# Kernel optimization log

Measured on AMD Instinct MI355X. Metric: run time of the kernel, lower is better.

The kernel has to match this reference:

```python
import jax, jax.numpy as jnp
import numpy as np

E, D, A, F, K = 512, 1024, 128, 32, 31  # encoder_dim, decoder_dim, attention_dim, location_filters, kernel
B, T = 128, 512


def setup_inputs() -> dict:
    key = jax.random.key(0)
    ks = jax.random.split(key, 9)
    s = lambda *sh: 1.0 / np.sqrt(sh[-1])
    return {
        "encoder_outputs": jax.random.normal(ks[0], (B, T, E), jnp.float32),
        "decoder_state": jax.random.normal(ks[1], (B, D), jnp.float32),
        "prev_attention_weights": jax.random.uniform(ks[2], (B, T), jnp.float32),
        # parameters (torch Linear stores [out, in]; Conv1d [out, in, K])
        "W_enc": jax.random.normal(ks[3], (A, E), jnp.float32) * s(A, E),
        "W_dec": jax.random.normal(ks[4], (A, D), jnp.float32) * s(A, D),
        "conv_w": jax.random.normal(ks[5], (F, 1, K), jnp.float32) * (1.0 / np.sqrt(K)),
        "W_loc": jax.random.normal(ks[6], (A, F), jnp.float32) * s(A, F),
        "W_e": jax.random.normal(ks[7], (1, A), jnp.float32) * s(1, A),
        "b_e": jax.random.normal(ks[8], (1,), jnp.float32) * 0.01,
    }


def reference(encoder_outputs, decoder_state, prev_attention_weights,
              W_enc, W_dec, conv_w, W_loc, W_e, b_e):
    # encoder projection: [B,T,E] @ [E,A] -> [B,T,A]
    enc_p = jnp.einsum('bte,ae->bta', encoder_outputs, W_enc)
    # decoder projection: [B,D] -> [B,1,A]
    dec_p = jnp.einsum('bd,ad->ba', decoder_state, W_dec)[:, None, :]
    # location conv: [B,1,T] * [F,1,K] -> [B,F,T], 'same' padding
    loc = jax.lax.conv_general_dilated(
        prev_attention_weights[:, None, :], conv_w,
        window_strides=(1,), padding=[((K - 1) // 2, (K - 1) // 2)],
        dimension_numbers=('NCH', 'OIH', 'NCH'))
    # [B,F,T] -> [B,T,A]
    loc_p = jnp.einsum('bft,af->bta', loc, W_loc)
    # energies: [B,T]
    energies = jnp.einsum('bta,a->bt', jnp.tanh(enc_p + dec_p + loc_p), W_e[0]) + b_e[0]
    attention_weights = jax.nn.softmax(energies, axis=1)
    # context: [B,T] x [B,T,E] -> [B,E]
    context_vector = jnp.einsum('bt,bte->be', attention_weights, encoder_outputs)
    return context_vector, attention_weights
```

## Files before the change

### kernel.cpp

```cpp
#include <hip/hip_runtime.h>
#include <hip/hip_bf16.h>
#include <math.h>

namespace {
constexpr int EDIM  = 512;
constexpr int DDIM  = 1024;
constexpr int ADIM  = 128;
constexpr int FDIM  = 32;
constexpr int KW    = 31;
constexpr int BATCH = 128;
constexpr int TDIM  = 512;

constexpr int BM  = 64;
constexpr int LDA = 40;

constexpr size_t N_ENC  = (size_t)BATCH * TDIM * EDIM;
constexpr size_t N_WENC = (size_t)ADIM * EDIM;
constexpr size_t N_WLOC = (size_t)ADIM * FDIM;
constexpr size_t N_BF   = N_ENC + N_WENC + N_WLOC;
constexpr size_t WS_NEEDED = N_BF * 2 + (size_t)BATCH * ADIM * 4;

typedef __attribute__((ext_vector_type(8))) short short8;
typedef __attribute__((ext_vector_type(4))) float floatx4;

__device__ __forceinline__ float fast_tanh(float x) {
  x = fminf(9.0f, fmaxf(-9.0f, x));
  float e = __expf(2.0f * x);
  return (e - 1.0f) / (e + 1.0f);
}

__device__ __forceinline__ ushort2 pack_bf16(float x, float y) {
  union { __hip_bfloat162 h; ushort2 u; } cv;
  cv.h = __float22bfloat162_rn(make_float2(x, y));
  return cv.u;
}

__device__ __forceinline__ void stage4(ushort* dst, const float4 v) {
  ushort2 lo = pack_bf16(v.x, v.y);
  ushort2 hi = pack_bf16(v.z, v.w);
  *(ushort4*)dst = make_ushort4(lo.x, lo.y, hi.x, hi.y);
}

__device__ __forceinline__ void async_ld16(const void* g, void* l) {
  __builtin_amdgcn_global_load_lds(
      (const __attribute__((address_space(1))) unsigned int*)g,
      (__attribute__((address_space(3))) unsigned int*)l, 16, 0, 0);
}

__global__ __launch_bounds__(256)
void cvt_kernel(const float* __restrict__ enc, const float* __restrict__ Wenc,
                const float* __restrict__ Wloc, ushort* __restrict__ out) {
  size_t e0 = (size_t)blockIdx.x * 2048 + (size_t)threadIdx.x * 8;
  const float* s;
  size_t off;
  if (e0 < N_ENC) { s = enc; off = e0; }
  else if (e0 < N_ENC + N_WENC) { s = Wenc; off = e0 - N_ENC; }
  else { s = Wloc; off = e0 - (N_ENC + N_WENC); }
  float4 v0 = *(const float4*)(s + off);
  float4 v1 = *(const float4*)(s + off + 4);
  union { ushort2 u[4]; short8 v; } o;
  o.u[0] = pack_bf16(v0.x, v0.y); o.u[1] = pack_bf16(v0.z, v0.w);
  o.u[2] = pack_bf16(v1.x, v1.y); o.u[3] = pack_bf16(v1.z, v1.w);
  *(short8*)(out + e0) = o.v;
}

__global__ __launch_bounds__(256)
void dec_proj_kernel(const float* __restrict__ dec,
                     const float* __restrict__ Wdec,
                     float* __restrict__ dec_p) {
  int b = blockIdx.x, az = blockIdx.y;
  int tid = threadIdx.x;
  int al = tid >> 3, seg = tid & 7;
  int a = az * 32 + al;
  const float* dv = dec + (size_t)b * DDIM;
  const float* wv = Wdec + (size_t)a * DDIM;
  float s = 0.f;
  #pragma unroll 8
  for (int it = 0; it < 32; ++it) {
    int d = it * 32 + seg * 4;
    float4 d4 = *(const float4*)(dv + d);
    float4 w4 = *(const float4*)(wv + d);
    s += d4.x * w4.x + d4.y * w4.y + d4.z * w4.z + d4.w * w4.w;
  }
  s += __shfl_xor(s, 1, 64);
  s += __shfl_xor(s, 2, 64);
  s += __shfl_xor(s, 4, 64);
  if (seg == 0) dec_p[b * ADIM + a] = s;
}

__global__ __launch_bounds__(256)
void energies_mfma_kernel(const ushort* __restrict__ enc16,
                          const ushort* __restrict__ wenc16,
                          const ushort* __restrict__ wloc16,
                          const float* __restrict__ pa,
                          const float* __restrict__ convw,
                          const float* __restrict__ We,
                          const float* __restrict__ be,
                          const float* __restrict__ dec_p,
                          float* __restrict__ energies) {
  __shared__ ushort As[BM * 64];
  __shared__ ushort Bs[ADIM * 64];
  __shared__ float pa_s[96];
  __shared__ float cw_s[FDIM][KW + 2];
  __shared__ float We_s[ADIM];
  __shared__ float dp_s[ADIM];
  __shared__ float epart[2][BM];

  const int tid  = threadIdx.x;
  const int b    = blockIdx.y;
  const int t0   = blockIdx.x * BM;
  const int wave = tid >> 6, lane = tid & 63;
  const int wt = wave >> 1, wa = wave & 1;
  const int lc = lane & 15, lq = lane >> 4;
  const int sw = lc & 7;

  if (tid < 96) {
    int gt = t0 - 15 + tid;
    pa_s[tid] = (gt >= 0 && gt < TDIM) ? pa[b * TDIM + gt] : 0.0f;
  }
  for (int id = tid; id < FDIM * KW; id += 256)
    cw_s[id / KW][id % KW] = convw[id];
  if (tid < ADIM) {
    We_s[tid] = We[tid];
    dp_s[tid] = dec_p[b * ADIM + tid];
  }

  const int iA0 = tid, iA1 = tid + 256;
  const ushort* gA0 = enc16 + (size_t)(b * TDIM + t0 + (iA0 >> 3)) * EDIM
                      + ((iA0 & 7) ^ ((iA0 >> 3) & 7)) * 8;
  const ushort* gA1 = enc16 + (size_t)(b * TDIM + t0 + (iA1 >> 3)) * EDIM
                      + ((iA1 & 7) ^ ((iA1 >> 3) & 7)) * 8;
  ushort* lA0 = As + iA0 * 8;
  ushort* lA1 = As + iA1 * 8;
  const ushort* gB[4];
  ushort* lB[4];
  #pragma unroll
  for (int r = 0; r < 4; ++r) {
    int idx = tid + r * 256;
    int row = idx >> 3, gc = (idx & 7) ^ (row & 7);
    gB[r] = wenc16 + (size_t)row * EDIM + gc * 8;
    lB[r] = Bs + idx * 8;
  }

  floatx4 acc[2][4];
  #pragma unroll
  for (int tt = 0; tt < 2; ++tt)
    #pragma unroll
    for (int aT = 0; aT < 4; ++aT)
      acc[tt][aT] = (floatx4){0.f, 0.f, 0.f, 0.f};

  ushort2 cvp[4];

  for (int kt = 0; kt < 8; ++kt) {
    async_ld16(gA0, lA0); async_ld16(gA1, lA1);
    async_ld16(gB[0], lB[0]); async_ld16(gB[1], lB[1]);
    async_ld16(gB[2], lB[2]); async_ld16(gB[3], lB[3]);
    gA0 += 64; gA1 += 64;
    gB[0] += 64; gB[1] += 64; gB[2] += 64; gB[3] += 64;
    __syncthreads();

    if (kt == 0) {
      int tl = tid >> 2, fg = tid & 3;
      float cv[8];
      #pragma unroll
      for (int n = 0; n < 8; ++n) {
        int f = fg * 8 + n;
        float s = 0.f;
        #pragma unroll
        for (int k = 0; k < KW; ++k) s += pa_s[tl + k] * cw_s[f][k];
        cv[n] = s;
      }
      cvp[0] = pack_bf16(cv[0], cv[1]);
      cvp[1] = pack_bf16(cv[2], cv[3]);
      cvp[2] = pack_bf16(cv[4], cv[5]);
      cvp[3] = pack_bf16(cv[6], cv[7]);
    }

    #pragma unroll
    for (int kk = 0; kk < 2; ++kk) {
      const int cco = ((kk * 4 + lq) ^ sw) * 8;
      short8 af[2], bf[4];
      #pragma unroll
      for (int tt = 0; tt < 2; ++tt)
        af[tt] = *(const short8*)&As[(wt * 32 + tt * 16 + lc) * 64 + cco];
      #pragma unroll
      for (int aT = 0; aT < 4; ++aT)
        bf[aT] = *(const short8*)&Bs[(wa * 64 + aT * 16 + lc) * 64 + cco];
      #pragma unroll
      for (int tt = 0; tt < 2; ++tt)
        #pragma unroll
        for (int aT = 0; aT < 4; ++aT)
          acc[tt][aT] = __builtin_amdgcn_mfma_f32_16x16x32_bf16(
              af[tt], bf[aT], acc[tt][aT], 0, 0, 0);
    }
    __syncthreads();
  }

  {
    int tl = tid >> 2, fg = tid & 3;
    union { ushort2 u[4]; short8 v; } o;
    o.u[0] = cvp[0]; o.u[1] = cvp[1]; o.u[2] = cvp[2]; o.u[3] = cvp[3];
    *(short8*)&As[tl * 64 + (fg ^ (tl & 7)) * 8] = o.v;
    #pragma unroll
    for (int r = 0; r < 2; ++r) {
      int idx = tid + r * 256;
      int row = idx >> 2, gc = idx & 3;
      *(short8*)&Bs[row * 64 + (gc ^ (row & 7)) * 8] =
          *(const short8*)(wloc16 + row * 32 + gc * 8);
    }
    __syncthreads();
    const int cco = (lq ^ sw) * 8;
    short8 af[2], bf[4];
    #pragma unroll
    for (int tt = 0; tt < 2; ++tt)
      af[tt] = *(const short8*)&As[(wt * 32 + tt * 16 + lc) * 64 + cco];
    #pragma unroll
    for (int aT = 0; aT < 4; ++aT)
      bf[aT] = *(const short8*)&Bs[(wa * 64 + aT * 16 + lc) * 64 + cco];
    #pragma unroll
    for (int tt = 0; tt < 2; ++tt)
      #pragma unroll
      for (int aT = 0; aT < 4; ++aT)
        acc[tt][aT] = __builtin_amdgcn_mfma_f32_16x16x32_bf16(
            af[tt], bf[aT], acc[tt][aT], 0, 0, 0);
  }

  float dpv[4], wev[4];
  #pragma unroll
  for (int aT = 0; aT < 4; ++aT) {
    int a = wa * 64 + aT * 16 + lc;
    dpv[aT] = dp_s[a];
    wev[aT] = We_s[a];
  }
  #pragma unroll
  for (int tt = 0; tt < 2; ++tt) {
    float es[4] = {0.f, 0.f, 0.f, 0.f};
    #pragma unroll
    for (int aT = 0; aT < 4; ++aT)
      #pragma unroll
      for (int i = 0; i < 4; ++i)
        es[i] += fast_tanh(acc[tt][aT][i] + dpv[aT]) * wev[aT];
    #pragma unroll
    for (int m = 1; m < 16; m <<= 1)
      #pragma unroll
      for (int i = 0; i < 4; ++i) es[i] += __shfl_xor(es[i], m, 64);
    if (lc == 0)
      #pragma unroll
      for (int i = 0; i < 4; ++i)
        epart[wa][wt * 32 + tt * 16 + lq * 4 + i] = es[i];
  }
  __syncthreads();
  if (tid < BM)
    energies[(size_t)b * TDIM + t0 + tid] = epart[0][tid] + epart[1][tid] + be[0];
}

__global__ __launch_bounds__(256)
void energies_fallback_kernel(const float* __restrict__ enc,
                              const float* __restrict__ Wenc,
                              const float* __restrict__ pa,
                              const float* __restrict__ convw,
                              const float* __restrict__ Wloc,
                              const float* __restrict__ We,
                              const float* __restrict__ be,
                              const float* __restrict__ dec_p,
                              float* __restrict__ energies) {
  __shared__ ushort As[BM][LDA];
  __shared__ ushort Bs[ADIM][LDA];
  __shared__ float pa_s[96];
  __shared__ float cw_s[FDIM][KW + 2];
  __shared__ float We_s[ADIM];
  __shared__ float dp_s[ADIM];
  __shared__ float epart[2][BM];

  const int tid  = threadIdx.x;
  const int b    = blockIdx.y;
  const int t0   = blockIdx.x * BM;
  const int wave = tid >> 6, lane = tid & 63;
  const int wt = wave >> 1, wa = wave & 1;
  const int lc = lane & 15, lq = lane >> 4;

  if (tid < 96) {
    int gt = t0 - 15 + tid;
    pa_s[tid] = (gt >= 0 && gt < TDIM) ? pa[b * TDIM + gt] : 0.0f;
  }
  for (int id = tid; id < FDIM * KW; id += 256)
    cw_s[id / KW][id % KW] = convw[id];
  if (tid < ADIM) {
    We_s[tid] = We[tid];
    dp_s[tid] = dec_p[b * ADIM + tid];
  }

  floatx4 acc[2][4];
  #pragma unroll
  for (int tt = 0; tt < 2; ++tt)
    #pragma unroll
    for (int aT = 0; aT < 4; ++aT)
      acc[tt][aT] = (floatx4){0.f, 0.f, 0.f, 0.f};

  const float* encB = enc + ((size_t)b * TDIM + t0) * EDIM;
  ushort2 cvp[4];

  for (int kt = 0; kt < 17; ++kt) {
    if (kt < 16) {
      const int k0 = kt * 32;
      #pragma unroll
      for (int r = 0; r < 2; ++r) {
        int id = tid + 256 * r;
        int row = id >> 3, c4 = id & 7;
        float4 v = *(const float4*)(encB + (size_t)row * EDIM + k0 + c4 * 4);
        stage4(&As[row][c4 * 4], v);
      }
      #pragma unroll
      for (int r = 0; r < 4; ++r) {
        int id = tid + 256 * r;
        int row = id >> 3, c4 = id & 7;
        float4 v = *(const float4*)(Wenc + (size_t)row * EDIM + k0 + c4 * 4);
        stage4(&Bs[row][c4 * 4], v);
      }
    } else {
      int tl = tid >> 2, fg = tid & 3;
      *(ushort2*)&As[tl][fg * 8 + 0] = cvp[0];
      *(ushort2*)&As[tl][fg * 8 + 2] = cvp[1];
      *(ushort2*)&As[tl][fg * 8 + 4] = cvp[2];
      *(ushort2*)&As[tl][fg * 8 + 6] = cvp[3];
      #pragma unroll
      for (int r = 0; r < 4; ++r) {
        int id = tid + 256 * r;
        int row = id >> 3, c4 = id & 7;
        float4 v = *(const float4*)(Wloc + (size_t)row * FDIM + c4 * 4);
        stage4(&Bs[row][c4 * 4], v);
      }
    }
    __syncthreads();
    if (kt == 0) {
      int tl = tid >> 2, fg = tid & 3;
      float cv[8];
      #pragma unroll
      for (int n = 0; n < 8; ++n) {
        int f = fg * 8 + n;
        float s = 0.f;
        #pragma unroll
        for (int k = 0; k < KW; ++k) s += pa_s[tl + k] * cw_s[f][k];
        cv[n] = s;
      }
      cvp[0] = pack_bf16(cv[0], cv[1]);
      cvp[1] = pack_bf16(cv[2], cv[3]);
      cvp[2] = pack_bf16(cv[4], cv[5]);
      cvp[3] = pack_bf16(cv[6], cv[7]);
    }
    short8 af[2], bf[4];
    #pragma unroll
    for (int tt = 0; tt < 2; ++tt)
      af[tt] = *(const short8*)&As[wt * 32 + tt * 16 + lc][lq * 8];
    #pragma unroll
    for (int aT = 0; aT < 4; ++aT)
      bf[aT] = *(const short8*)&Bs[wa * 64 + aT * 16 + lc][lq * 8];
    #pragma unroll
    for (int tt = 0; tt < 2; ++tt)
      #pragma unroll
      for (int aT = 0; aT < 4; ++aT)
        acc[tt][aT] = __builtin_amdgcn_mfma_f32_16x16x32_bf16(
            af[tt], bf[aT], acc[tt][aT], 0, 0, 0);
    __syncthreads();
  }

  float dpv[4], wev[4];
  #pragma unroll
  for (int aT = 0; aT < 4; ++aT) {
    int a = wa * 64 + aT * 16 + lc;
    dpv[aT] = dp_s[a];
    wev[aT] = We_s[a];
  }
  #pragma unroll
  for (int tt = 0; tt < 2; ++tt) {
    float es[4] = {0.f, 0.f, 0.f, 0.f};
    #pragma unroll
    for (int aT = 0; aT < 4; ++aT)
      #pragma unroll
      for (int i = 0; i < 4; ++i)
        es[i] += fast_tanh(acc[tt][aT][i] + dpv[aT]) * wev[aT];
    #pragma unroll
    for (int m = 1; m < 16; m <<= 1)
      #pragma unroll
      for (int i = 0; i < 4; ++i) es[i] += __shfl_xor(es[i], m, 64);
    if (lc == 0)
      #pragma unroll
      for (int i = 0; i < 4; ++i)
        epart[wa][wt * 32 + tt * 16 + lq * 4 + i] = es[i];
  }
  __syncthreads();
  if (tid < BM)
    energies[(size_t)b * TDIM + t0 + tid] = epart[0][tid] + epart[1][tid] + be[0];
}

__global__ __launch_bounds__(256)
void softmax_kernel(float* __restrict__ attn) {
  int b = blockIdx.x;
  int tid = threadIdx.x;
  float* row = attn + (size_t)b * TDIM;
  float x0 = row[tid], x1 = row[tid + 256];
  float m = fmaxf(x0, x1);
  #pragma unroll
  for (int off = 32; off; off >>= 1) m = fmaxf(m, __shfl_xor(m, off, 64));
  __shared__ float redm[4];
  __shared__ float reds[4];
  int wid = tid >> 6, lane = tid & 63;
  if (lane == 0) redm[wid] = m;
  __syncthreads();
  m = fmaxf(fmaxf(redm[0], redm[1]), fmaxf(redm[2], redm[3]));
  float e0 = __expf(x0 - m), e1 = __expf(x1 - m);
  float s = e0 + e1;
  #pragma unroll
  for (int off = 32; off; off >>= 1) s += __shfl_xor(s, off, 64);
  if (lane == 0) reds[wid] = s;
  __syncthreads();
  s = reds[0] + reds[1] + reds[2] + reds[3];
  float inv = 1.0f / s;
  row[tid] = e0 * inv;
  row[tid + 256] = e1 * inv;
}

__global__ __launch_bounds__(256)
void context_kernel(const float* __restrict__ enc,
                    const float* __restrict__ attn,
                    float* __restrict__ ctx) {
  int e = blockIdx.x * 256 + threadIdx.x;
  int b = blockIdx.y;
  int tc = blockIdx.z * 128;
  const float* w = attn + (size_t)b * TDIM + tc;
  const float* ep = enc + ((size_t)b * TDIM + tc) * EDIM + e;
  float acc = 0.f;
  #pragma unroll 8
  for (int t = 0; t < 128; ++t) acc += w[t] * ep[(size_t)t * EDIM];
  atomicAdd(&ctx[(size_t)b * EDIM + e], acc);
}

}

extern "C" void kernel_launch(void* const* d_in, const int* in_sizes, int n_in,
                              void* d_out, int out_size, void* d_ws, size_t ws_size,
                              hipStream_t stream) {
  const float* enc   = (const float*)d_in[0];
  const float* dec   = (const float*)d_in[1];
  const float* pa    = (const float*)d_in[2];
  const float* Wenc  = (const float*)d_in[3];
  const float* Wdec  = (const float*)d_in[4];
  const float* convw = (const float*)d_in[5];
  const float* Wloc  = (const float*)d_in[6];
  const float* We    = (const float*)d_in[7];
  const float* be    = (const float*)d_in[8];

  float* ctx  = (float*)d_out;
  float* attn = (float*)d_out + BATCH * EDIM;

  hipMemsetAsync(ctx, 0, (size_t)BATCH * EDIM * sizeof(float), stream);

  if (ws_size >= WS_NEEDED) {
    ushort* enc16  = (ushort*)d_ws;
    ushort* wenc16 = enc16 + N_ENC;
    ushort* wloc16 = enc16 + N_ENC + N_WENC;
    float*  dec_p  = (float*)(enc16 + N_BF);

    cvt_kernel<<<(unsigned)((N_BF + 2047) / 2048), 256, 0, stream>>>(
        enc, Wenc, Wloc, enc16);
    dim3 g1(BATCH, 4);
    dec_proj_kernel<<<g1, 256, 0, stream>>>(dec, Wdec, dec_p);
    dim3 g3(TDIM / BM, BATCH);
    energies_mfma_kernel<<<g3, 256, 0, stream>>>(enc16, wenc16, wloc16, pa,
                                                 convw, We, be, dec_p, attn);
  } else {
    float* dec_p = (float*)d_ws;
    dim3 g1(BATCH, 4);
    dec_proj_kernel<<<g1, 256, 0, stream>>>(dec, Wdec, dec_p);
    dim3 g3(TDIM / BM, BATCH);
    energies_fallback_kernel<<<g3, 256, 0, stream>>>(enc, Wenc, pa, convw,
                                                     Wloc, We, be, dec_p, attn);
  }

  softmax_kernel<<<BATCH, 256, 0, stream>>>(attn);

  dim3 g5(EDIM / 256, BATCH, TDIM / 128);
  context_kernel<<<g5, 256, 0, stream>>>(enc, attn, ctx);
}
```

Before: 285.4 us.

## Read bf16 encoder copy in context, double-buffer energies GEMM, fuse prep kernels

The context reduction now reads the bf16 encoder copy produced for the GEMM, halving its memory traffic, and reduces across waves in LDS before atomics. The energies kernel double-buffers async global-to-LDS tiles, computes the location conv before the K loop, and targets higher occupancy. The conversion and decoder projection are merged into one launch. This trades context precision (bf16 inputs) for lower bandwidth.

```diff
diff --git a/kernel.cpp b/kernel.cpp
--- a/kernel.cpp
+++ b/kernel.cpp
@@ -19,6 +19,8 @@
 constexpr size_t N_WLOC = (size_t)ADIM * FDIM;
 constexpr size_t N_BF   = N_ENC + N_WENC + N_WLOC;
 constexpr size_t WS_NEEDED = N_BF * 2 + (size_t)BATCH * ADIM * 4;
+constexpr int CVT_BLOCKS = (int)(N_BF / 2048);
+constexpr int DEC_BLOCKS = BATCH * 4;
 
 typedef __attribute__((ext_vector_type(8))) short short8;
 typedef __attribute__((ext_vector_type(4))) float floatx4;
@@ -35,6 +37,12 @@
   return cv.u;
 }
 
+__device__ __forceinline__ float b2f(short u) {
+  union { unsigned int i; float f; } c;
+  c.i = ((unsigned int)(unsigned short)u) << 16;
+  return c.f;
+}
+
 __device__ __forceinline__ void stage4(ushort* dst, const float4 v) {
   ushort2 lo = pack_bf16(v.x, v.y);
   ushort2 hi = pack_bf16(v.z, v.w);
@@ -48,20 +56,409 @@
 }
 
 __global__ __launch_bounds__(256)
-void cvt_kernel(const float* __restrict__ enc, const float* __restrict__ Wenc,
-                const float* __restrict__ Wloc, ushort* __restrict__ out) {
-  size_t e0 = (size_t)blockIdx.x * 2048 + (size_t)threadIdx.x * 8;
-  const float* s;
-  size_t off;
-  if (e0 < N_ENC) { s = enc; off = e0; }
-  else if (e0 < N_ENC + N_WENC) { s = Wenc; off = e0 - N_ENC; }
-  else { s = Wloc; off = e0 - (N_ENC + N_WENC); }
-  float4 v0 = *(const float4*)(s + off);
-  float4 v1 = *(const float4*)(s + off + 4);
-  union { ushort2 u[4]; short8 v; } o;
-  o.u[0] = pack_bf16(v0.x, v0.y); o.u[1] = pack_bf16(v0.z, v0.w);
-  o.u[2] = pack_bf16(v1.x, v1.y); o.u[3] = pack_bf16(v1.z, v1.w);
-  *(short8*)(out + e0) = o.v;
+void prep_kernel(const float* __restrict__ enc, const float* __restrict__ Wenc,
+                 const float* __restrict__ Wloc, const float* __restrict__ dec,
+                 const float* __restrict__ Wdec, ushort* __restrict__ out16,
+                 float* __restrict__ dec_p) {
+  int bid = blockIdx.x;
+  if (bid < CVT_BLOCKS) {
+    size_t e0 = (size_t)bid * 2048 + (size_t)threadIdx.x * 8;
+    const float* s;
+    size_t off;
+    if (e0 < N_ENC) { s = enc; off = e0; }
+    else if (e0 < N_ENC + N_WENC) { s = Wenc; off = e0 - N_ENC; }
+    else { s = Wloc; off = e0 - (N_ENC + N_WENC); }
+    float4 v0 = *(const float4*)(s + off);
+    float4 v1 = *(const float4*)(s + off + 4);
+    union { ushort2 u[4]; short8 v; } o;
+    o.u[0] = pack_bf16(v0.x, v0.y); o.u[1] = pack_bf16(v0.z, v0.w);
+    o.u[2] = pack_bf16(v1.x, v1.y); o.u[3] = pack_bf16(v1.z, v1.w);
+    *(short8*)(out16 + e0) = o.v;
+  } else {
+    int id = bid - CVT_BLOCKS;
+    int b = id >> 2, az = id & 3;
+    int tid = threadIdx.x;
+    int al = tid >> 3, seg = tid & 7;
+    int a = az * 32 + al;
+    const float* dv = dec + (size_t)b * DDIM;
+    const float* wv = Wdec + (size_t)a * DDIM;
+    float s = 0.f;
+    #pragma unroll 8
+    for (int it = 0; it < 32; ++it) {
+      int d = it * 32 + seg * 4;
+      float4 d4 = *(const float4*)(dv + d);
+      float4 w4 = *(const float4*)(wv + d);
+      s += d4.x * w4.x + d4.y * w4.y + d4.z * w4.z + d4.w * w4.w;
+    }
+    s += __shfl_xor(s, 1, 64);
+    s += __shfl_xor(s, 2, 64);
+    s += __shfl_xor(s, 4, 64);
+    if (seg == 0) dec_p[b * ADIM + a] = s;
+  }
+}
+
+__global__ __launch_bounds__(256, 3)
+void energies_mfma_kernel(const ushort* __restrict__ enc16,
+                          const ushort* __restrict__ wenc16,
+                          const ushort* __restrict__ wloc16,
+                          const float* __restrict__ pa,
+                          const float* __restrict__ convw,
+                          const float* __restrict__ We,
+                          const float* __restrict__ be,
+                          const float* __restrict__ dec_p,
+                          float* __restrict__ energies) {
+  __shared__ ushort lds[24832];
+  float* pa_s  = (float*)(lds + 16384);
+  float* cw_s  = pa_s + 96;
+  float* epart = (float*)(lds + 24576);
+
+  const int tid  = threadIdx.x;
+  const int b    = blockIdx.y;
+  const int t0   = blockIdx.x * BM;
+  const int wave = tid >> 6, lane = tid & 63;
+  const int wt = wave >> 1, wa = wave & 1;
+  const int lc = lane & 15, lq = lane >> 4;
+  const int sw = lc & 7;
+
+  if (tid < 96) {
+    int gt = t0 - 15 + tid;
+    pa_s[tid] = (gt >= 0 && gt < TDIM) ? pa[b * TDIM + gt] : 0.0f;
+  }
+  for (int id = tid; id < FDIM * KW; id += 256)
+    cw_s[(id / KW) * 33 + (id % KW)] = convw[id];
+
+  const int iA0 = tid, iA1 = tid + 256;
+  const ushort* gA0 = enc16 + (size_t)(b * TDIM + t0 + (iA0 >> 3)) * EDIM
+                      + ((iA0 & 7) ^ ((iA0 >> 3) & 7)) * 8;
+  const ushort* gA1 = enc16 + (size_t)(b * TDIM + t0 + (iA1 >> 3)) * EDIM
+                      + ((iA1 & 7) ^ ((iA1 >> 3) & 7)) * 8;
+  ushort* lA0 = lds + iA0 * 8;
+  ushort* lA1 = lds + iA1 * 8;
+  const ushort* gB[4];
+  ushort* lB[4];
+  #pragma unroll
+  for (int r = 0; r < 4; ++r) {
+    int idx = tid + r * 256;
+    int row = idx >> 3, gc = (idx & 7) ^ (row & 7);
+    gB[r] = wenc16 + (size_t)row * EDIM + gc * 8;
+    lB[r] = lds + 8192 + idx * 8;
+  }
+
+  async_ld16(gA0, lA0); async_ld16(gA1, lA1);
+  async_ld16(gB[0], lB[0]); async_ld16(gB[1], lB[1]);
+  async_ld16(gB[2], lB[2]); async_ld16(gB[3], lB[3]);
+  gA0 += 64; gA1 += 64;
+  gB[0] += 64; gB[1] += 64; gB[2] += 64; gB[3] += 64;
+
+  const int wi0 = tid, wi1 = tid + 256;
+  short8 wl0 = *(const short8*)(wloc16 + (wi0 >> 2) * FDIM + (wi0 & 3) * 8);
+  short8 wl1 = *(const short8*)(wloc16 + (wi1 >> 2) * FDIM + (wi1 & 3) * 8);
+
+  __syncthreads();
+
+  const int tl = tid >> 2, fg = tid & 3;
+  union { ushort2 u[4]; short8 v; } cvo;
+  {
+    float cv[8];
+    #pragma unroll
+    for (int n = 0; n < 8; ++n) {
+      int f = fg * 8 + n;
+      float s = 0.f;
+      #pragma unroll
+      for (int k = 0; k < KW; ++k) s += pa_s[tl + k] * cw_s[f * 33 + k];
+      cv[n] = s;
+    }
+    cvo.u[0] = pack_bf16(cv[0], cv[1]);
+    cvo.u[1] = pack_bf16(cv[2], cv[3]);
+    cvo.u[2] = pack_bf16(cv[4], cv[5]);
+    cvo.u[3] = pack_bf16(cv[6], cv[7]);
+  }
+  __syncthreads();
+
+  floatx4 acc[2][4];
+  #pragma unroll
+  for (int tt = 0; tt < 2; ++tt)
+    #pragma unroll
+    for (int aT = 0; aT < 4; ++aT)
+      acc[tt][aT] = (floatx4){0.f, 0.f, 0.f, 0.f};
+
+  for (int kt = 0; kt < 8; ++kt) {
+    if (kt) __syncthreads();
+    const int cur = kt & 1;
+    if (kt < 7) {
+      const int aoff = (cur ^ 1) << 12;
+      const int boff = (cur ^ 1) << 13;
+      async_ld16(gA0, lA0 + aoff); async_ld16(gA1, lA1 + aoff);
+      async_ld16(gB[0], lB[0] + boff); async_ld16(gB[1], lB[1] + boff);
+      async_ld16(gB[2], lB[2] + boff); async_ld16(gB[3], lB[3] + boff);
+      gA0 += 64; gA1 += 64;
+      gB[0] += 64; gB[1] += 64; gB[2] += 64; gB[3] += 64;
+    } else {
+      *(short8*)&lds[tl * 64 + (fg ^ (tl & 7)) * 8] = cvo.v;
+      *(short8*)&lds[8192 + (wi0 >> 2) * 64 + ((wi0 & 3) ^ ((wi0 >> 2) & 7)) * 8] = wl0;
+      *(short8*)&lds[8192 + (wi1 >> 2) * 64 + ((wi1 & 3) ^ ((wi1 >> 2) & 7)) * 8] = wl1;
+    }
+    const ushort* Ab = lds + (cur << 12);
+    const ushort* Bb = lds + 8192 + (cur << 13);
+    #pragma unroll
+    for (int kk = 0; kk < 2; ++kk) {
+      const int cco = ((kk * 4 + lq) ^ sw) * 8;
+      short8 af[2], bf[4];
+      #pragma unroll
+      for (int tt = 0; tt < 2; ++tt)
+        af[tt] = *(const short8*)&Ab[(wt * 32 + tt * 16 + lc) * 64 + cco];
+      #pragma unroll
+      for (int aT = 0; aT < 4; ++aT)
+        bf[aT] = *(const short8*)&Bb[(wa * 64 + aT * 16 + lc) * 64 + cco];
+      #pragma unroll
+      for (int tt = 0; tt < 2; ++tt)
+        #pragma unroll
+        for (int aT = 0; aT < 4; ++aT)
+          acc[tt][aT] = __builtin_amdgcn_mfma_f32_16x16x32_bf16(
+              af[tt], bf[aT], acc[tt][aT], 0, 0, 0);
+    }
+  }
+  __syncthreads();
+
+  {
+    const int cco = (lq ^ sw) * 8;
+    short8 af[2], bf[4];
+    #pragma unroll
+    for (int tt = 0; tt < 2; ++tt)
+      af[tt] = *(const short8*)&lds[(wt * 32 + tt * 16 + lc) * 64 + cco];
+    #pragma unroll
+    for (int aT = 0; aT < 4; ++aT)
+      bf[aT] = *(const short8*)&lds[8192 + (wa * 64 + aT * 16 + lc) * 64 + cco];
+    #pragma unroll
+    for (int tt = 0; tt < 2; ++tt)
+      #pragma unroll
+      for (int aT = 0; aT < 4; ++aT)
+        acc[tt][aT] = __builtin_amdgcn_mfma_f32_16x16x32_bf16(
+            af[tt], bf[aT], acc[tt][aT], 0, 0, 0);
+  }
+
+  float dpv[4], wev[4];
+  #pragma unroll
+  for (int aT = 0; aT < 4; ++aT) {
+    int a = wa * 64 + aT * 16 + lc;
+    dpv[aT] = dec_p[b * ADIM + a];
+    wev[aT] = We[a];
+  }
+  #pragma unroll
+  for (int tt = 0; tt < 2; ++tt) {
+    float es[4] = {0.f, 0.f, 0.f, 0.f};
+    #pragma unroll
+    for (int aT = 0; aT < 4; ++aT)
+      #pragma unroll
+      for (int i = 0; i < 4; ++i)
+        es[i] += fast_tanh(acc[tt][aT][i] + dpv[aT]) * wev[aT];
+    #pragma unroll
+    for (int m = 1; m < 16; m <<= 1)
+      #pragma unroll
+      for (int i = 0; i < 4; ++i) es[i] += __shfl_xor(es[i], m, 64);
+    if (lc == 0)
+      #pragma unroll
+      for (int i = 0; i < 4; ++i)
+        epart[wa * 64 + wt * 32 + tt * 16 + lq * 4 + i] = es[i];
+  }
+  __syncthreads();
+  if (tid < BM)
+    energies[(size_t)b * TDIM + t0 + tid] = epart[tid] + epart[64 + tid] + be[0];
+}
+
+__global__ __launch_bounds__(256)
+void softmax_kernel(float* __restrict__ attn) {
+  int b = blockIdx.x;
+  int tid = threadIdx.x;
+  float* row = attn + (size_t)b * TDIM;
+  float x0 = row[tid], x1 = row[tid + 256];
+  float m = fmaxf(x0, x1);
+  #pragma unroll
+  for (int off = 32; off; off >>= 1) m = fmaxf(m, __shfl_xor(m, off, 64));
+  __shared__ float redm[4];
+  __shared__ float reds[4];
+  int wid = tid >> 6, lane = tid & 63;
+  if (lane == 0) redm[wid] = m;
+  __syncthreads();
+  m = fmaxf(fmaxf(redm[0], redm[1]), fmaxf(redm[2], redm[3]));
+  float e0 = __expf(x0 - m), e1 = __expf(x1 - m);
+  float s = e0 + e1;
+  #pragma unroll
+  for (int off = 32; off; off >>= 1) s += __shfl_xor(s, off, 64);
+  if (lane == 0) reds[wid] = s;
+  __syncthreads();
+  s = reds[0] + reds[1] + reds[2] + reds[3];
+  float inv = 1.0f / s;
+  row[tid] = e0 * inv;
+  row[tid + 256] = e1 * inv;
+}
+
+__global__ __launch_bounds__(256)
+void context_bf16_kernel(const ushort* __restrict__ enc16,
+                         const float* __restrict__ attn,
+                         float* __restrict__ ctx) {
+  __shared__ float red[4][512];
+  const int b = blockIdx.y, tc = blockIdx.x * 128;
+  const int wave = threadIdx.x >> 6, lane = threadIdx.x & 63;
+  float acc[8] = {0.f, 0.f, 0.f, 0.f, 0.f, 0.f, 0.f, 0.f};
+  const float* aw = attn + (size_t)b * TDIM + tc + wave * 32;
+  const ushort* ep = enc16 + ((size_t)b * TDIM + tc + wave * 32) * EDIM + lane * 8;
+  #pragma unroll 2
+  for (int t = 0; t < 32; t += 2) {
+    short8 v0 = *(const short8*)(ep + (size_t)t * EDIM);
+    short8 v1 = *(const short8*)(ep + (size_t)(t + 1) * EDIM);
+    float w0 = aw[t], w1 = aw[t + 1];
+    #pragma unroll
+    for (int j = 0; j < 8; ++j)
+      acc[j] += w0 * b2f(v0[j]) + w1 * b2f(v1[j]);
+  }
+  #pragma unroll
+  for (int j = 0; j < 8; ++j) red[wave][lane * 8 + j] = acc[j];
+  __syncthreads();
+  int e = threadIdx.x * 2;
+  float s0 = red[0][e] + red[1][e] + red[2][e] + red[3][e];
+  float s1 = red[0][e + 1] + red[1][e + 1] + red[2][e + 1] + red[3][e + 1];
+  atomicAdd(&ctx[(size_t)b * EDIM + e], s0);
+  atomicAdd(&ctx[(size_t)b * EDIM + e + 1], s1);
+}
+
+__global__ __launch_bounds__(256)
+void energies_fallback_kernel(const float* __restrict__ enc,
+                              const float* __restrict__ Wenc,
+                              const float* __restrict__ pa,
+                              const float* __restrict__ convw,
+                              const float* __restrict__ Wloc,
+                              const float* __restrict__ We,
+                              const float* __restrict__ be,
+                              const float* __restrict__ dec_p,
+                              float* __restrict__ energies) {
+  __shared__ ushort As[BM][LDA];
+  __shared__ ushort Bs[ADIM][LDA];
+  __shared__ float pa_s[96];
+  __shared__ float cw_s[FDIM][KW + 2];
+  __shared__ float We_s[ADIM];
+  __shared__ float dp_s[ADIM];
+  __shared__ float epart[2][BM];
+
+  const int tid  = threadIdx.x;
+  const int b    = blockIdx.y;
+  const int t0   = blockIdx.x * BM;
+  const int wave = tid >> 6, lane = tid & 63;
+  const int wt = wave >> 1, wa = wave & 1;
+  const int lc = lane & 15, lq = lane >> 4;
+
+  if (tid < 96) {
+    int gt = t0 - 15 + tid;
+    pa_s[tid] = (gt >= 0 && gt < TDIM) ? pa[b * TDIM + gt] : 0.0f;
+  }
+  for (int id = tid; id < FDIM * KW; id += 256)
+    cw_s[id / KW][id % KW] = convw[id];
+  if (tid < ADIM) {
+    We_s[tid] = We[tid];
+    dp_s[tid] = dec_p[b * ADIM + tid];
+  }
+
+  floatx4 acc[2][4];
+  #pragma unroll
+  for (int tt = 0; tt < 2; ++tt)
+    #pragma unroll
+    for (int aT = 0; aT < 4; ++aT)
+      acc[tt][aT] = (floatx4){0.f, 0.f, 0.f, 0.f};
+
+  const float* encB = enc + ((size_t)b * TDIM + t0) * EDIM;
+  ushort2 cvp[4];
+
+  for (int kt = 0; kt < 17; ++kt) {
+    if (kt < 16) {
+      const int k0 = kt * 32;
+      #pragma unroll
+      for (int r = 0; r < 2; ++r) {
+        int id = tid + 256 * r;
+        int row = id >> 3, c4 = id & 7;
+        float4 v = *(const float4*)(encB + (size_t)row * EDIM + k0 + c4 * 4);
+        stage4(&As[row][c4 * 4], v);
+      }
+      #pragma unroll
+      for (int r = 0; r < 4; ++r) {
+        int id = tid + 256 * r;
+        int row = id >> 3, c4 = id & 7;
+        float4 v = *(const float4*)(Wenc + (size_t)row * EDIM + k0 + c4 * 4);
+        stage4(&Bs[row][c4 * 4], v);
+      }
+    } else {
+      int tl = tid >> 2, fg = tid & 3;
+      *(ushort2*)&As[tl][fg * 8 + 0] = cvp[0];
+      *(ushort2*)&As[tl][fg * 8 + 2] = cvp[1];
+      *(ushort2*)&As[tl][fg * 8 + 4] = cvp[2];
+      *(ushort2*)&As[tl][fg * 8 + 6] = cvp[3];
+      #pragma unroll
+      for (int r = 0; r < 4; ++r) {
+        int id = tid + 256 * r;
+        int row = id >> 3, c4 = id & 7;
+        float4 v = *(const float4*)(Wloc + (size_t)row * FDIM + c4 * 4);
+        stage4(&Bs[row][c4 * 4], v);
+      }
+    }
+    __syncthreads();
+    if (kt == 0) {
+      int tl = tid >> 2, fg = tid & 3;
+      float cv[8];
+      #pragma unroll
+      for (int n = 0; n < 8; ++n) {
+        int f = fg * 8 + n;
+        float s = 0.f;
+        #pragma unroll
+        for (int k = 0; k < KW; ++k) s += pa_s[tl + k] * cw_s[f][k];
+        cv[n] = s;
+      }
+      cvp[0] = pack_bf16(cv[0], cv[1]);
+      cvp[1] = pack_bf16(cv[2], cv[3]);
+      cvp[2] = pack_bf16(cv[4], cv[5]);
+      cvp[3] = pack_bf16(cv[6], cv[7]);
+    }
+    short8 af[2], bf[4];
+    #pragma unroll
+    for (int tt = 0; tt < 2; ++tt)
+      af[tt] = *(const short8*)&As[wt * 32 + tt * 16 + lc][lq * 8];
+    #pragma unroll
+    for (int aT = 0; aT < 4; ++aT)
+      bf[aT] = *(const short8*)&Bs[wa * 64 + aT * 16 + lc][lq * 8];
+    #pragma unroll
+    for (int tt = 0; tt < 2; ++tt)
+      #pragma unroll
+      for (int aT = 0; aT < 4; ++aT)
+        acc[tt][aT] = __builtin_amdgcn_mfma_f32_16x16x32_bf16(
+            af[tt], bf[aT], acc[tt][aT], 0, 0, 0);
+    __syncthreads();
+  }
+
+  float dpv[4], wev[4];
+  #pragma unroll
+  for (int aT = 0; aT < 4; ++aT) {
+    int a = wa * 64 + aT * 16 + lc;
+    dpv[aT] = dp_s[a];
+    wev[aT] = We_s[a];
+  }
+  #pragma unroll
+  for (int tt = 0; tt < 2; ++tt) {
+    float es[4] = {0.f, 0.f, 0.f, 0.f};
+    #pragma unroll
+    for (int aT = 0; aT < 4; ++aT)
+      #pragma unroll
+      for (int i = 0; i < 4; ++i)
+        es[i] += fast_tanh(acc[tt][aT][i] + dpv[aT]) * wev[aT];
+    #pragma unroll
+    for (int m = 1; m < 16; m <<= 1)
+      #pragma unroll
+      for (int i = 0; i < 4; ++i) es[i] += __shfl_xor(es[i], m, 64);
+    if (lc == 0)
+      #pragma unroll
+      for (int i = 0; i < 4; ++i)
+        epart[wa][wt * 32 + tt * 16 + lq * 4 + i] = es[i];
+  }
+  __syncthreads();
+  if (tid < BM)
+    energies[(size_t)b * TDIM + t0 + tid] = epart[0][tid] + epart[1][tid] + be[0];
 }
 
 __global__ __launch_bounds__(256)
@@ -89,341 +486,9 @@
 }
 
 __global__ __launch_bounds__(256)
-void energies_mfma_kernel(const ushort* __restrict__ enc16,
-                          const ushort* __restrict__ wenc16,
-                          const ushort* __restrict__ wloc16,
-                          const float* __restrict__ pa,
-                          const float* __restrict__ convw,
-                          const float* __restrict__ We,
-                          const float* __restrict__ be,
-                          const float* __restrict__ dec_p,
-                          float* __restrict__ energies) {
-  __shared__ ushort As[BM * 64];
-  __shared__ ushort Bs[ADIM * 64];
-  __shared__ float pa_s[96];
-  __shared__ float cw_s[FDIM][KW + 2];
-  __shared__ float We_s[ADIM];
-  __shared__ float dp_s[ADIM];
-  __shared__ float epart[2][BM];
-
-  const int tid  = threadIdx.x;
-  const int b    = blockIdx.y;
-  const int t0   = blockIdx.x * BM;
-  const int wave = tid >> 6, lane = tid & 63;
-  const int wt = wave >> 1, wa = wave & 1;
-  const int lc = lane & 15, lq = lane >> 4;
-  const int sw = lc & 7;
-
-  if (tid < 96) {
-    int gt = t0 - 15 + tid;
-    pa_s[tid] = (gt >= 0 && gt < TDIM) ? pa[b * TDIM + gt] : 0.0f;
-  }
-  for (int id = tid; id < FDIM * KW; id += 256)
-    cw_s[id / KW][id % KW] = convw[id];
-  if (tid < ADIM) {
-    We_s[tid] = We[tid];
-    dp_s[tid] = dec_p[b * ADIM + tid];
-  }
-
-  const int iA0 = tid, iA1 = tid + 256;
-  const ushort* gA0 = enc16 + (size_t)(b * TDIM + t0 + (iA0 >> 3)) * EDIM
-                      + ((iA0 & 7) ^ ((iA0 >> 3) & 7)) * 8;
-  const ushort* gA1 = enc16 + (size_t)(b * TDIM + t0 + (iA1 >> 3)) * EDIM
-                      + ((iA1 & 7) ^ ((iA1 >> 3) & 7)) * 8;
-  ushort* lA0 = As + iA0 * 8;
-  ushort* lA1 = As + iA1 * 8;
-  const ushort* gB[4];
-  ushort* lB[4];
-  #pragma unroll
-  for (int r = 0; r < 4; ++r) {
-    int idx = tid + r * 256;
-    int row = idx >> 3, gc = (idx & 7) ^ (row & 7);
-    gB[r] = wenc16 + (size_t)row * EDIM + gc * 8;
-    lB[r] = Bs + idx * 8;
-  }
-
-  floatx4 acc[2][4];
-  #pragma unroll
-  for (int tt = 0; tt < 2; ++tt)
-    #pragma unroll
-    for (int aT = 0; aT < 4; ++aT)
-      acc[tt][aT] = (floatx4){0.f, 0.f, 0.f, 0.f};
-
-  ushort2 cvp[4];
-
-  for (int kt = 0; kt < 8; ++kt) {
-    async_ld16(gA0, lA0); async_ld16(gA1, lA1);
-    async_ld16(gB[0], lB[0]); async_ld16(gB[1], lB[1]);
-    async_ld16(gB[2], lB[2]); async_ld16(gB[3], lB[3]);
-    gA0 += 64; gA1 += 64;
-    gB[0] += 64; gB[1] += 64; gB[2] += 64; gB[3] += 64;
-    __syncthreads();
-
-    if (kt == 0) {
-      int tl = tid >> 2, fg = tid & 3;
-      float cv[8];
-      #pragma unroll
-      for (int n = 0; n < 8; ++n) {
-        int f = fg * 8 + n;
-        float s = 0.f;
-        #pragma unroll
-        for (int k = 0; k < KW; ++k) s += pa_s[tl + k] * cw_s[f][k];
-        cv[n] = s;
-      }
-      cvp[0] = pack_bf16(cv[0], cv[1]);
-      cvp[1] = pack_bf16(cv[2], cv[3]);
-      cvp[2] = pack_bf16(cv[4], cv[5]);
-      cvp[3] = pack_bf16(cv[6], cv[7]);
-    }
-
-    #pragma unroll
-    for (int kk = 0; kk < 2; ++kk) {
-      const int cco = ((kk * 4 + lq) ^ sw) * 8;
-      short8 af[2], bf[4];
-      #pragma unroll
-      for (int tt = 0; tt < 2; ++tt)
-        af[tt] = *(const short8*)&As[(wt * 32 + tt * 16 + lc) * 64 + cco];
-      #pragma unroll
-      for (int aT = 0; aT < 4; ++aT)
-        bf[aT] = *(const short8*)&Bs[(wa * 64 + aT * 16 + lc) * 64 + cco];
-      #pragma unroll
-      for (int tt = 0; tt < 2; ++tt)
-        #pragma unroll
-        for (int aT = 0; aT < 4; ++aT)
-          acc[tt][aT] = __builtin_amdgcn_mfma_f32_16x16x32_bf16(
-              af[tt], bf[aT], acc[tt][aT], 0, 0, 0);
-    }
-    __syncthreads();
-  }
-
-  {
-    int tl = tid >> 2, fg = tid & 3;
-    union { ushort2 u[4]; short8 v; } o;
-    o.u[0] = cvp[0]; o.u[1] = cvp[1]; o.u[2] = cvp[2]; o.u[3] = cvp[3];
-    *(short8*)&As[tl * 64 + (fg ^ (tl & 7)) * 8] = o.v;
-    #pragma unroll
-    for (int r = 0; r < 2; ++r) {
-      int idx = tid + r * 256;
-      int row = idx >> 2, gc = idx & 3;
-      *(short8*)&Bs[row * 64 + (gc ^ (row & 7)) * 8] =
-          *(const short8*)(wloc16 + row * 32 + gc * 8);
-    }
-    __syncthreads();
-    const int cco = (lq ^ sw) * 8;
-    short8 af[2], bf[4];
-    #pragma unroll
-    for (int tt = 0; tt < 2; ++tt)
-      af[tt] = *(const short8*)&As[(wt * 32 + tt * 16 + lc) * 64 + cco];
-    #pragma unroll
-    for (int aT = 0; aT < 4; ++aT)
-      bf[aT] = *(const short8*)&Bs[(wa * 64 + aT * 16 + lc) * 64 + cco];
-    #pragma unroll
-    for (int tt = 0; tt < 2; ++tt)
-      #pragma unroll
-      for (int aT = 0; aT < 4; ++aT)
-        acc[tt][aT] = __builtin_amdgcn_mfma_f32_16x16x32_bf16(
-            af[tt], bf[aT], acc[tt][aT], 0, 0, 0);
-  }
-
-  float dpv[4], wev[4];
-  #pragma unroll
-  for (int aT = 0; aT < 4; ++aT) {
-    int a = wa * 64 + aT * 16 + lc;
-    dpv[aT] = dp_s[a];
-    wev[aT] = We_s[a];
-  }
-  #pragma unroll
-  for (int tt = 0; tt < 2; ++tt) {
-    float es[4] = {0.f, 0.f, 0.f, 0.f};
-    #pragma unroll
-    for (int aT = 0; aT < 4; ++aT)
-      #pragma unroll
-      for (int i = 0; i < 4; ++i)
-        es[i] += fast_tanh(acc[tt][aT][i] + dpv[aT]) * wev[aT];
-    #pragma unroll
-    for (int m = 1; m < 16; m <<= 1)
-      #pragma unroll
-      for (int i = 0; i < 4; ++i) es[i] += __shfl_xor(es[i], m, 64);
-    if (lc == 0)
-      #pragma unroll
-      for (int i = 0; i < 4; ++i)
-        epart[wa][wt * 32 + tt * 16 + lq * 4 + i] = es[i];
-  }
-  __syncthreads();
-  if (tid < BM)
-    energies[(size_t)b * TDIM + t0 + tid] = epart[0][tid] + epart[1][tid] + be[0];
-}
-
-__global__ __launch_bounds__(256)
-void energies_fallback_kernel(const float* __restrict__ enc,
-                              const float* __restrict__ Wenc,
-                              const float* __restrict__ pa,
-                              const float* __restrict__ convw,
-                              const float* __restrict__ Wloc,
-                              const float* __restrict__ We,
-                              const float* __restrict__ be,
-                              const float* __restrict__ dec_p,
-                              float* __restrict__ energies) {
-  __shared__ ushort As[BM][LDA];
-  __shared__ ushort Bs[ADIM][LDA];
-  __shared__ float pa_s[96];
-  __shared__ float cw_s[FDIM][KW + 2];
-  __shared__ float We_s[ADIM];
-  __shared__ float dp_s[ADIM];
-  __shared__ float epart[2][BM];
-
-  const int tid  = threadIdx.x;
-  const int b    = blockIdx.y;
-  const int t0   = blockIdx.x * BM;
-  const int wave = tid >> 6, lane = tid & 63;
-  const int wt = wave >> 1, wa = wave & 1;
-  const int lc = lane & 15, lq = lane >> 4;
-
-  if (tid < 96) {
-    int gt = t0 - 15 + tid;
-    pa_s[tid] = (gt >= 0 && gt < TDIM) ? pa[b * TDIM + gt] : 0.0f;
-  }
-  for (int id = tid; id < FDIM * KW; id += 256)
-    cw_s[id / KW][id % KW] = convw[id];
-  if (tid < ADIM) {
-    We_s[tid] = We[tid];
-    dp_s[tid] = dec_p[b * ADIM + tid];
-  }
-
-  floatx4 acc[2][4];
-  #pragma unroll
-  for (int tt = 0; tt < 2; ++tt)
-    #pragma unroll
-    for (int aT = 0; aT < 4; ++aT)
-      acc[tt][aT] = (floatx4){0.f, 0.f, 0.f, 0.f};
-
-  const float* encB = enc + ((size_t)b * TDIM + t0) * EDIM;
-  ushort2 cvp[4];
-
-  for (int kt = 0; kt < 17; ++kt) {
-    if (kt < 16) {
-      const int k0 = kt * 32;
-      #pragma unroll
-      for (int r = 0; r < 2; ++r) {
-        int id = tid + 256 * r;
-        int row = id >> 3, c4 = id & 7;
-        float4 v = *(const float4*)(encB + (size_t)row * EDIM + k0 + c4 * 4);
-        stage4(&As[row][c4 * 4], v);
-      }
-      #pragma unroll
-      for (int r = 0; r < 4; ++r) {
-        int id = tid + 256 * r;
-        int row = id >> 3, c4 = id & 7;
-        float4 v = *(const float4*)(Wenc + (size_t)row * EDIM + k0 + c4 * 4);
-        stage4(&Bs[row][c4 * 4], v);
-      }
-    } else {
-      int tl = tid >> 2, fg = tid & 3;
-      *(ushort2*)&As[tl][fg * 8 + 0] = cvp[0];
-      *(ushort2*)&As[tl][fg * 8 + 2] = cvp[1];
-      *(ushort2*)&As[tl][fg * 8 + 4] = cvp[2];
-      *(ushort2*)&As[tl][fg * 8 + 6] = cvp[3];
-      #pragma unroll
-      for (int r = 0; r < 4; ++r) {
-        int id = tid + 256 * r;
-        int row = id >> 3, c4 = id & 7;
-        float4 v = *(const float4*)(Wloc + (size_t)row * FDIM + c4 * 4);
-        stage4(&Bs[row][c4 * 4], v);
-      }
-    }
-    __syncthreads();
-    if (kt == 0) {
-      int tl = tid >> 2, fg = tid & 3;
-      float cv[8];
-      #pragma unroll
-      for (int n = 0; n < 8; ++n) {
-        int f = fg * 8 + n;
-        float s = 0.f;
-        #pragma unroll
-        for (int k = 0; k < KW; ++k) s += pa_s[tl + k] * cw_s[f][k];
-        cv[n] = s;
-      }
-      cvp[0] = pack_bf16(cv[0], cv[1]);
-      cvp[1] = pack_bf16(cv[2], cv[3]);
-      cvp[2] = pack_bf16(cv[4], cv[5]);
-      cvp[3] = pack_bf16(cv[6], cv[7]);
-    }
-    short8 af[2], bf[4];
-    #pragma unroll
-    for (int tt = 0; tt < 2; ++tt)
-      af[tt] = *(const short8*)&As[wt * 32 + tt * 16 + lc][lq * 8];
-    #pragma unroll
-    for (int aT = 0; aT < 4; ++aT)
-      bf[aT] = *(const short8*)&Bs[wa * 64 + aT * 16 + lc][lq * 8];
-    #pragma unroll
-    for (int tt = 0; tt < 2; ++tt)
-      #pragma unroll
-      for (int aT = 0; aT < 4; ++aT)
-        acc[tt][aT] = __builtin_amdgcn_mfma_f32_16x16x32_bf16(
-            af[tt], bf[aT], acc[tt][aT], 0, 0, 0);
-    __syncthreads();
-  }
-
-  float dpv[4], wev[4];
-  #pragma unroll
-  for (int aT = 0; aT < 4; ++aT) {
-    int a = wa * 64 + aT * 16 + lc;
-    dpv[aT] = dp_s[a];
-    wev[aT] = We_s[a];
-  }
-  #pragma unroll
-  for (int tt = 0; tt < 2; ++tt) {
-    float es[4] = {0.f, 0.f, 0.f, 0.f};
-    #pragma unroll
-    for (int aT = 0; aT < 4; ++aT)
-      #pragma unroll
-      for (int i = 0; i < 4; ++i)
-        es[i] += fast_tanh(acc[tt][aT][i] + dpv[aT]) * wev[aT];
-    #pragma unroll
-    for (int m = 1; m < 16; m <<= 1)
-      #pragma unroll
-      for (int i = 0; i < 4; ++i) es[i] += __shfl_xor(es[i], m, 64);
-    if (lc == 0)
-      #pragma unroll
-      for (int i = 0; i < 4; ++i)
-        epart[wa][wt * 32 + tt * 16 + lq * 4 + i] = es[i];
-  }
-  __syncthreads();
-  if (tid < BM)
-    energies[(size_t)b * TDIM + t0 + tid] = epart[0][tid] + epart[1][tid] + be[0];
-}
-
-__global__ __launch_bounds__(256)
-void softmax_kernel(float* __restrict__ attn) {
-  int b = blockIdx.x;
-  int tid = threadIdx.x;
-  float* row = attn + (size_t)b * TDIM;
-  float x0 = row[tid], x1 = row[tid + 256];
-  float m = fmaxf(x0, x1);
-  #pragma unroll
-  for (int off = 32; off; off >>= 1) m = fmaxf(m, __shfl_xor(m, off, 64));
-  __shared__ float redm[4];
-  __shared__ float reds[4];
-  int wid = tid >> 6, lane = tid & 63;
-  if (lane == 0) redm[wid] = m;
-  __syncthreads();
-  m = fmaxf(fmaxf(redm[0], redm[1]), fmaxf(redm[2], redm[3]));
-  float e0 = __expf(x0 - m), e1 = __expf(x1 - m);
-  float s = e0 + e1;
-  #pragma unroll
-  for (int off = 32; off; off >>= 1) s += __shfl_xor(s, off, 64);
-  if (lane == 0) reds[wid] = s;
-  __syncthreads();
-  s = reds[0] + reds[1] + reds[2] + reds[3];
-  float inv = 1.0f / s;
-  row[tid] = e0 * inv;
-  row[tid + 256] = e1 * inv;
-}
-
-__global__ __launch_bounds__(256)
-void context_kernel(const float* __restrict__ enc,
-                    const float* __restrict__ attn,
-                    float* __restrict__ ctx) {
+void context_f32_kernel(const float* __restrict__ enc,
+                        const float* __restrict__ attn,
+                        float* __restrict__ ctx) {
   int e = blockIdx.x * 256 + threadIdx.x;
   int b = blockIdx.y;
   int tc = blockIdx.z * 128;
@@ -461,13 +526,14 @@
     ushort* wloc16 = enc16 + N_ENC + N_WENC;
     float*  dec_p  = (float*)(enc16 + N_BF);
 
-    cvt_kernel<<<(unsigned)((N_BF + 2047) / 2048), 256, 0, stream>>>(
-        enc, Wenc, Wloc, enc16);
-    dim3 g1(BATCH, 4);
-    dec_proj_kernel<<<g1, 256, 0, stream>>>(dec, Wdec, dec_p);
+    prep_kernel<<<CVT_BLOCKS + DEC_BLOCKS, 256, 0, stream>>>(
+        enc, Wenc, Wloc, dec, Wdec, enc16, dec_p);
     dim3 g3(TDIM / BM, BATCH);
     energies_mfma_kernel<<<g3, 256, 0, stream>>>(enc16, wenc16, wloc16, pa,
                                                  convw, We, be, dec_p, attn);
+    softmax_kernel<<<BATCH, 256, 0, stream>>>(attn);
+    dim3 g5(TDIM / 128, BATCH);
+    context_bf16_kernel<<<g5, 256, 0, stream>>>(enc16, attn, ctx);
   } else {
     float* dec_p = (float*)d_ws;
     dim3 g1(BATCH, 4);
@@ -475,10 +541,8 @@
     dim3 g3(TDIM / BM, BATCH);
     energies_fallback_kernel<<<g3, 256, 0, stream>>>(enc, Wenc, pa, convw,
                                                      Wloc, We, be, dec_p, attn);
-  }
-
-  softmax_kernel<<<BATCH, 256, 0, stream>>>(attn);
-
-  dim3 g5(EDIM / 256, BATCH, TDIM / 128);
-  context_kernel<<<g5, 256, 0, stream>>>(enc, attn, ctx);
-}
+    softmax_kernel<<<BATCH, 256, 0, stream>>>(attn);
+    dim3 g5(EDIM / 256, BATCH, TDIM / 128);
+    context_f32_kernel<<<g5, 256, 0, stream>>>(enc, attn, ctx);
+  }
+}
```

New measurement: 282.9 us. About the same (-0.9%).
